# Optimization experiments

Hardware: AMD Instinct MI355X
Metric: run time of the kernel (lower is better)

The kernel has to match this reference:

```python
import jax, jax.numpy as jnp
import numpy as np

B, TQ, TK, DQ, DK = 8, 2048, 2048, 512, 512


def setup_inputs() -> dict:
    key = jax.random.key(0)
    kq, kk, kv, km, kw = jax.random.split(key, 5)
    q = jax.random.normal(kq, (B, TQ, DQ), dtype=jnp.float32)
    k = jax.random.normal(kk, (B, TK, DK), dtype=jnp.float32)
    v = jax.random.normal(kv, (B, TK, DK), dtype=jnp.float32)
    attn_mask = jax.random.randint(km, (B, TQ, TK), 0, 2) > 0
    # xavier_uniform for (DQ, DK)
    limit = float(np.sqrt(6.0 / (DQ + DK)))
    weights = jax.random.uniform(kw, (DQ, DK), minval=-limit, maxval=limit, dtype=jnp.float32)
    return {"q": q, "k": k, "v": v, "attn_mask": attn_mask, "weights": weights}


def reference(q, k, v, attn_mask, weights):
    # scores: (B, TQ, TK) = (q @ W) @ k^T
    qw = jnp.einsum('bqd,de->bqe', q, weights)
    scores = jnp.einsum('bqe,bke->bqk', qw, k)
    scores = jnp.where(attn_mask, -jnp.inf, scores)
    attention = jax.nn.softmax(scores, axis=-1)
    # dropout_rate = 0.0 -> identity
    output = jnp.einsum('bqk,bkd->bqd', attention, v)
    return (output, attention)
```

## Files before the change

### kernel.cpp

```cpp
#include <hip/hip_runtime.h>
#include <stdint.h>

#define TQs 2048
#define TKs 2048
#define DDs 512
#define NBs 8

typedef float f32x4 __attribute__((ext_vector_type(4)));
typedef float f32x2 __attribute__((ext_vector_type(2)));
typedef short bf16x8 __attribute__((ext_vector_type(8)));
typedef short bf16x4 __attribute__((ext_vector_type(4)));
typedef short bf16x2 __attribute__((ext_vector_type(2)));
typedef _Float16 half8 __attribute__((ext_vector_type(8)));

__device__ __forceinline__ unsigned short f2bf(float x){
  unsigned u = __float_as_uint(x);
  return (unsigned short)((u + 0x7fffu + ((u>>16)&1u)) >> 16);
}
__device__ __forceinline__ float bf2f(unsigned short h){
  return __uint_as_float(((unsigned)h)<<16);
}

__device__ __forceinline__ void gload16(const void* g, void* l){
  __builtin_amdgcn_global_load_lds(
      (const __attribute__((address_space(1))) unsigned int*)(unsigned long long)(uintptr_t)g,
      (__attribute__((address_space(3))) unsigned int*)(unsigned int)(uintptr_t)l,
      16, 0, 0);
}

__global__ __launch_bounds__(256) void k0_kf(const float* __restrict__ kk, _Float16* __restrict__ kf){
  const long n8 = (long)NBs*TKs*DDs/8;
  for(long i = (long)blockIdx.x*256 + threadIdx.x; i < n8; i += (long)gridDim.x*256){
    f32x4 x0 = ((const f32x4*)kk)[2*i];
    f32x4 x1 = ((const f32x4*)kk)[2*i+1];
    half8 h;
    #pragma unroll
    for(int j=0;j<4;j++){ h[j] = (_Float16)x0[j]; h[4+j] = (_Float16)x1[j]; }
    ((half8*)kf)[i] = h;
  }
}

__global__ __launch_bounds__(256) void k0_transpose_v(const float* __restrict__ v, short* __restrict__ vt){
  __shared__ float tile[64][65];
  int b = blockIdx.z;
  int t0 = blockIdx.x*64, d0 = blockIdx.y*64;
  int tid = threadIdx.x;
  int r = tid>>2, cs = (tid&3)*16;
  const float* src = v + ((long)b*TKs + t0 + r)*DDs + d0 + cs;
  #pragma unroll
  for(int i=0;i<4;i++){
    f32x4 x = ((const f32x4*)src)[i];
    tile[r][cs+4*i+0]=x[0]; tile[r][cs+4*i+1]=x[1]; tile[r][cs+4*i+2]=x[2]; tile[r][cs+4*i+3]=x[3];
  }
  __syncthreads();
  int dr = tid>>2, ts = (tid&3)*16;
  bf16x8 b0, b1;
  #pragma unroll
  for(int i=0;i<8;i++){ b0[i] = (short)f2bf(tile[ts+i][dr]); b1[i] = (short)f2bf(tile[ts+8+i][dr]); }
  short* dst = vt + ((long)b*DDs + d0 + dr)*TKs + t0 + ts;
  ((bf16x8*)dst)[0] = b0;
  ((bf16x8*)dst)[1] = b1;
}

__global__ __launch_bounds__(256) void k0_wt(const float* __restrict__ wsrc,
                                             short* __restrict__ wth, short* __restrict__ wtl){
  __shared__ float tile[64][65];
  int d0 = blockIdx.x*64, e0 = blockIdx.y*64;
  int tid = threadIdx.x;
  int r = tid>>2, cs = (tid&3)*16;
  const float* src = wsrc + ((long)(d0 + r))*DDs + e0 + cs;
  #pragma unroll
  for(int i=0;i<4;i++){
    f32x4 x = ((const f32x4*)src)[i];
    tile[r][cs+4*i+0]=x[0]; tile[r][cs+4*i+1]=x[1]; tile[r][cs+4*i+2]=x[2]; tile[r][cs+4*i+3]=x[3];
  }
  __syncthreads();
  int er = tid>>2, ds = (tid&3)*16;
  bf16x8 h0,h1,l0,l1;
  #pragma unroll
  for(int i=0;i<8;i++){
    float x = tile[ds+i][er];
    unsigned short hh = f2bf(x);
    h0[i] = (short)hh; l0[i] = (short)f2bf(x - bf2f(hh));
  }
  #pragma unroll
  for(int i=0;i<8;i++){
    float x = tile[ds+8+i][er];
    unsigned short hh = f2bf(x);
    h1[i] = (short)hh; l1[i] = (short)f2bf(x - bf2f(hh));
  }
  short* dh = wth + ((long)(e0+er))*DDs + d0 + ds;
  short* dl = wtl + ((long)(e0+er))*DDs + d0 + ds;
  ((bf16x8*)dh)[0] = h0; ((bf16x8*)dh)[1] = h1;
  ((bf16x8*)dl)[0] = l0; ((bf16x8*)dl)[1] = l1;
}

__global__ __launch_bounds__(256,2) void k1_qw(const float* __restrict__ q,
                                               const short* __restrict__ wth, const short* __restrict__ wtl,
                                               _Float16* __restrict__ qwh, _Float16* __restrict__ qwl){
  __shared__ short qah[8192], qal[8192];
  __shared__ short wbh[8192], wbl[8192];
  int q0 = blockIdx.x*128, e0 = blockIdx.y*128;
  int tid = threadIdx.x, lane = tid&63, w4 = tid>>6;
  int wm = w4>>1, wn = w4&1;
  int i15 = lane&15, g4 = lane>>4;
  f32x4 acc[4][4];
  #pragma unroll
  for(int a=0;a<4;a++)
    #pragma unroll
    for(int bq=0;bq<4;bq++) acc[a][bq] = (f32x4){0.f,0.f,0.f,0.f};
  for(int k0=0;k0<DDs;k0+=64){
    __syncthreads();
    #pragma unroll
    for(int j=0;j<4;j++){
      int J = j*4 + w4;
      long so = (long)(e0 + (J>>1)*16 + i15)*DDs + k0 + ((J&1)*4 + g4)*8;
      gload16(wth + so, &wbh[J*512]);
      gload16(wtl + so, &wbl[J*512]);
    }
    #pragma unroll
    for(int j=0;j<4;j++){
      int c = j*256 + tid;
      int ci = c&15, cg = (c>>4)&3, cks = (c>>6)&1, crb = c>>7;
      const float* s = q + (long)(q0 + crb*16 + ci)*DDs + k0 + (cks*4+cg)*8;
      f32x4 x0 = ((const f32x4*)s)[0];
      f32x4 x1 = ((const f32x4*)s)[1];
      bf16x8 h, l;
      #pragma unroll
      for(int jj=0;jj<4;jj++){
        unsigned short hj = f2bf(x0[jj]);
        h[jj] = (short)hj; l[jj] = (short)f2bf(x0[jj]-bf2f(hj));
      }
      #pragma unroll
      for(int jj=0;jj<4;jj++){
        unsigned short hj = f2bf(x1[jj]);
        h[4+jj] = (short)hj; l[4+jj] = (short)f2bf(x1[jj]-bf2f(hj));
      }
      *(bf16x8*)&qah[c*8] = h;
      *(bf16x8*)&qal[c*8] = l;
    }
    __syncthreads();
    #pragma unroll
    for(int ks=0;ks<2;ks++){
      bf16x8 a_h[4], a_l[4], b_h[4], b_l[4];
      #pragma unroll
      for(int mf=0;mf<4;mf++){
        int c = ((wm*4+mf)*2+ks)*64 + lane;
        a_h[mf] = *(const bf16x8*)&qah[c*8];
        a_l[mf] = *(const bf16x8*)&qal[c*8];
      }
      #pragma unroll
      for(int nf=0;nf<4;nf++){
        int c = ((wn*4+nf)*2+ks)*64 + lane;
        b_h[nf] = *(const bf16x8*)&wbh[c*8];
        b_l[nf] = *(const bf16x8*)&wbl[c*8];
      }
      #pragma unroll
      for(int mf=0;mf<4;mf++)
      #pragma unroll
      for(int nf=0;nf<4;nf++){
        acc[mf][nf] = __builtin_amdgcn_mfma_f32_16x16x32_bf16(a_h[mf], b_h[nf], acc[mf][nf],0,0,0);
        acc[mf][nf] = __builtin_amdgcn_mfma_f32_16x16x32_bf16(a_h[mf], b_l[nf], acc[mf][nf],0,0,0);
        acc[mf][nf] = __builtin_amdgcn_mfma_f32_16x16x32_bf16(a_l[mf], b_h[nf], acc[mf][nf],0,0,0);
      }
    }
  }
  int rr = g4*4, cc = i15;
  #pragma unroll
  for(int mf=0;mf<4;mf++)
  #pragma unroll
  for(int nf=0;nf<4;nf++)
  #pragma unroll
  for(int r2=0;r2<4;r2++){
    long row = q0 + wm*64 + mf*16 + rr + r2;
    long col = e0 + wn*64 + nf*16 + cc;
    float s = acc[mf][nf][r2];
    _Float16 h = (_Float16)s;
    qwh[row*DDs + col] = h;
    qwl[row*DDs + col] = (_Float16)(s - (float)h);
  }
}

__global__ __launch_bounds__(256,2) void k2a(const _Float16* __restrict__ qwh, const _Float16* __restrict__ qwl,
                                             const _Float16* __restrict__ kf,
                                             const int* __restrict__ mask, float* __restrict__ attn,
                                             float* __restrict__ m_ws, float* __restrict__ l_ws){
  __shared__ _Float16 kb[2][16384];
  int rb = blockIdx.x;
  int chunk = blockIdx.y;
  int tid = threadIdx.x, lane = tid&63, w = tid>>6;
  int b = rb>>5;
  long qrow0 = (long)rb*64 + w*16;
  int i15 = lane&15, g4 = lane>>4;
  half8 ah[16], al[16];
  {
    const _Float16* ph = qwh + (qrow0 + i15)*DDs + g4*8;
    const _Float16* pl = qwl + (qrow0 + i15)*DDs + g4*8;
    #pragma unroll
    for(int kc=0;kc<16;kc++){
      ah[kc] = *(const half8*)(ph + kc*32);
      al[kc] = *(const half8*)(pl + kc*32);
    }
  }
  float m_st[4], l_st[4];
  #pragma unroll
  for(int r=0;r<4;r++){ m_st[r]=-1e30f; l_st[r]=0.f; }
  const _Float16* kbase = kf + (long)b*TKs*DDs;
  {
    int t0 = chunk*1024;
    #pragma unroll
    for(int j=0;j<8;j++){
      int J = j*4 + w;
      long so = (long)(t0 + ((J>>4)<<4) + i15)*DDs + (J&15)*32 + g4*8;
      gload16(kbase + so, &kb[0][J*512]);
    }
  }
  __syncthreads();
  int cur = 0;
  for(int it=0; it<32; ++it){
    int t0 = chunk*1024 + it*32;
    if(it < 31){
      int t1 = t0 + 32;
      #pragma unroll
      for(int j=0;j<8;j++){
        int J = j*4 + w;
        long so = (long)(t1 + ((J>>4)<<4) + i15)*DDs + (J&15)*32 + g4*8;
        gload16(kbase + so, &kb[cur^1][J*512]);
      }
    }
    int mv[2][4];
    #pragma unroll
    for(int nf=0;nf<2;nf++)
      #pragma unroll
      for(int r=0;r<4;r++)
        mv[nf][r] = mask[(qrow0 + g4*4 + r)*TKs + t0 + nf*16 + i15];
    f32x4 acc[2];
    acc[0]=(f32x4){0.f,0.f,0.f,0.f}; acc[1]=(f32x4){0.f,0.f,0.f,0.f};
    #pragma unroll
    for(int ks=0;ks<16;ks++){
      #pragma unroll
      for(int nf=0;nf<2;nf++){
        half8 bh = *(const half8*)&kb[cur][((nf*16+ks)*64 + lane)*8];
        acc[nf] = __builtin_amdgcn_mfma_f32_16x16x32_f16(ah[ks], bh, acc[nf],0,0,0);
        acc[nf] = __builtin_amdgcn_mfma_f32_16x16x32_f16(al[ks], bh, acc[nf],0,0,0);
      }
    }
    #pragma unroll
    for(int r=0;r<4;r++){
      float s0 = acc[0][r];
      float s1 = acc[1][r];
      if(mv[0][r]) s0 = -3e38f;
      if(mv[1][r]) s1 = -3e38f;
      float mo = m_st[r];
      float mn = fmaxf(mo, fmaxf(s0,s1));
      l_st[r] = l_st[r]*__expf(mo-mn) + __expf(s0-mn) + __expf(s1-mn);
      m_st[r] = mn;
      long row = qrow0 + g4*4 + r;
      attn[row*TKs + t0 + i15] = s0;
      attn[row*TKs + t0 + 16 + i15] = s1;
    }
    __syncthreads();
    cur ^= 1;
  }
  #pragma unroll
  for(int r=0;r<4;r++){
    #pragma unroll
    for(int d=1; d<16; d<<=1){
      float m2 = __shfl_xor(m_st[r], d, 16);
      float l2 = __shfl_xor(l_st[r], d, 16);
      float mn = fmaxf(m_st[r], m2);
      l_st[r] = l_st[r]*__expf(m_st[r]-mn) + l2*__expf(m2-mn);
      m_st[r] = mn;
    }
  }
  if(i15==0){
    #pragma unroll
    for(int r=0;r<4;r++){
      long row = qrow0 + g4*4 + r;
      m_ws[row*2 + chunk] = m_st[r];
      l_ws[row*2 + chunk] = l_st[r];
    }
  }
}

__global__ __launch_bounds__(512,4) void k2b(const short* __restrict__ vt, const float* __restrict__ m_ws,
                                             const float* __restrict__ l_ws, float* __restrict__ attn,
                                             float* __restrict__ outp){
  __shared__ short vf[2][16384];
  __shared__ short at2[2][1024];
  __shared__ float ms[32], rls[32];
  int rb = blockIdx.x;
  long row0 = (long)rb*32;
  int b = rb>>6;
  int tid=threadIdx.x, lane=tid&63, w=tid>>6;
  int i15 = lane&15, g4 = lane>>4;
  const short* vb = vt + (long)b*DDs*TKs;
  float* arow = attn + row0*TKs;
  int nr = tid>>4, nt = (tid&15)*2;
  int nmf = nr>>4, nrow = nr&15, ntg = nt>>3, nj = nt&7;
  int ncell = (nmf*64 + ntg*16 + nrow)*8 + nj;
  #pragma unroll
  for(int j=0;j<4;j++){
    int J = j*8 + w;
    long so = (long)(J*16 + i15)*TKs + g4*8;
    gload16(vb + so, &vf[0][J*512]);
  }
  if(tid < 32){
    long row = row0 + tid;
    float m0=m_ws[row*2+0], m1=m_ws[row*2+1];
    float M = fmaxf(m0,m1);
    float L = l_ws[row*2+0]*__expf(m0-M) + l_ws[row*2+1]*__expf(m1-M);
    ms[tid] = M;
    rls[tid] = 1.0f/L;
  }
  __syncthreads();
  {
    float* p = arow + (long)nr*TKs + nt;
    f32x2 s = *(const f32x2*)p;
    float M = ms[nr], RL = rls[nr];
    float a0 = __expf(s[0]-M)*RL, a1 = __expf(s[1]-M)*RL;
    f32x2 av; av[0]=a0; av[1]=a1;
    *(f32x2*)p = av;
    bf16x2 ab; ab[0]=(short)f2bf(a0); ab[1]=(short)f2bf(a1);
    *(bf16x2*)&at2[0][ncell] = ab;
  }
  __syncthreads();
  f32x4 acc[2][4];
  #pragma unroll
  for(int mf=0;mf<2;mf++)
    #pragma unroll
    for(int nf=0;nf<4;nf++) acc[mf][nf]=(f32x4){0.f,0.f,0.f,0.f};
  int c = 0;
  for(int it=0; it<64; ++it){
    float sx, sy;
    if(it < 63){
      int t1 = (it+1)*32;
      #pragma unroll
      for(int j=0;j<4;j++){
        int J = j*8 + w;
        long so = (long)(J*16 + i15)*TKs + t1 + g4*8;
        gload16(vb + so, &vf[c^1][J*512]);
      }
      const float* p = arow + (long)nr*TKs + t1 + nt;
      f32x2 s = *(const f32x2*)p;
      sx = s[0]; sy = s[1];
    }
    bf16x8 af[2], bfr[4];
    #pragma unroll
    for(int mf=0;mf<2;mf++) af[mf] = *(const bf16x8*)&at2[c][(mf*64 + lane)*8];
    #pragma unroll
    for(int nf=0;nf<4;nf++) bfr[nf] = *(const bf16x8*)&vf[c][((w*4+nf)*64 + lane)*8];
    #pragma unroll
    for(int mf=0;mf<2;mf++)
    #pragma unroll
    for(int nf=0;nf<4;nf++)
      acc[mf][nf] = __builtin_amdgcn_mfma_f32_16x16x32_bf16(af[mf], bfr[nf], acc[mf][nf],0,0,0);
    if(it < 63){
      int t1 = (it+1)*32;
      float* p = arow + (long)nr*TKs + t1 + nt;
      float M = ms[nr], RL = rls[nr];
      float a0 = __expf(sx-M)*RL, a1 = __expf(sy-M)*RL;
      f32x2 av; av[0]=a0; av[1]=a1;
      *(f32x2*)p = av;
      bf16x2 ab; ab[0]=(short)f2bf(a0); ab[1]=(short)f2bf(a1);
      *(bf16x2*)&at2[c^1][ncell] = ab;
    }
    __syncthreads();
    c ^= 1;
  }
  #pragma unroll
  for(int mf=0;mf<2;mf++)
  #pragma unroll
  for(int nf=0;nf<4;nf++)
  #pragma unroll
  for(int r2=0;r2<4;r2++){
    long row = row0 + mf*16 + g4*4 + r2;
    long col = w*64 + nf*16 + i15;
    outp[row*DDs + col] = acc[mf][nf][r2];
  }
}

extern "C" void kernel_launch(void* const* d_in, const int* in_sizes, int n_in,
                              void* d_out, int out_size, void* d_ws, size_t ws_size,
                              hipStream_t stream) {
  const float* q    = (const float*)d_in[0];
  const float* k    = (const float*)d_in[1];
  const float* v    = (const float*)d_in[2];
  const int*   mask = (const int*)d_in[3];
  const float* wsrc = (const float*)d_in[4];
  float* outp = (float*)d_out;
  float* attn = (float*)d_out + (long)NBs*TQs*DDs;
  char* ws = (char*)d_ws;
  const long NE = (long)NBs*TKs*DDs;
  _Float16* kf  = (_Float16*)ws;
  short*    vt  = (short*)(ws + 2*NE);
  _Float16* qwh = (_Float16*)(ws + 4*NE);
  _Float16* qwl = (_Float16*)(ws + 6*NE);
  float* m_ws = (float*)(ws + 8*NE);
  float* l_ws = (float*)(ws + 8*NE + 65536*4);
  short* wth = (short*)attn;
  short* wtl = (short*)attn + 262144;
  hipLaunchKernelGGL(k0_kf,          dim3(1024),    dim3(256), 0, stream, k, kf);
  hipLaunchKernelGGL(k0_transpose_v, dim3(32,8,8),  dim3(256), 0, stream, v, vt);
  hipLaunchKernelGGL(k0_wt,          dim3(8,8),     dim3(256), 0, stream, wsrc, wth, wtl);
  hipLaunchKernelGGL(k1_qw,          dim3(128,4),   dim3(256), 0, stream, q, wth, wtl, qwh, qwl);
  hipLaunchKernelGGL(k2a,            dim3(256,2),   dim3(256), 0, stream, qwh, qwl, kf, mask, attn, m_ws, l_ws);
  hipLaunchKernelGGL(k2b,            dim3(512),     dim3(512), 0, stream, vt, m_ws, l_ws, attn, outp);
}
```

Before: 354.3 us.

## Prefetch mask and score tiles one iteration ahead and remap normalize threads

In the score kernel, the boolean mask values for the next K tile are loaded one iteration early into registers, so the mask read latency overlaps the MFMA work. In the normalize/PV kernel, the raw score pair for tile it+2 is prefetched into registers, which moves the global load off the critical path. The thread-to-element mapping is also changed so each wave writes a contiguous LDS region in the MFMA A-operand layout via a byte offset, replacing the scattered cell index. These changes cost extra registers and could lower occupancy.

```diff
diff --git a/kernel.cpp b/kernel.cpp
--- a/kernel.cpp
+++ b/kernel.cpp
@@ -206,6 +206,7 @@
   #pragma unroll
   for(int r=0;r<4;r++){ m_st[r]=-1e30f; l_st[r]=0.f; }
   const _Float16* kbase = kf + (long)b*TKs*DDs;
+  int mv_pf[2][4];
   {
     int t0 = chunk*1024;
     #pragma unroll
@@ -214,6 +215,11 @@
       long so = (long)(t0 + ((J>>4)<<4) + i15)*DDs + (J&15)*32 + g4*8;
       gload16(kbase + so, &kb[0][J*512]);
     }
+    #pragma unroll
+    for(int nf=0;nf<2;nf++)
+      #pragma unroll
+      for(int r=0;r<4;r++)
+        mv_pf[nf][r] = mask[(qrow0 + g4*4 + r)*TKs + t0 + nf*16 + i15];
   }
   __syncthreads();
   int cur = 0;
@@ -233,7 +239,15 @@
     for(int nf=0;nf<2;nf++)
       #pragma unroll
       for(int r=0;r<4;r++)
-        mv[nf][r] = mask[(qrow0 + g4*4 + r)*TKs + t0 + nf*16 + i15];
+        mv[nf][r] = mv_pf[nf][r];
+    if(it < 31){
+      int t1 = t0 + 32;
+      #pragma unroll
+      for(int nf=0;nf<2;nf++)
+        #pragma unroll
+        for(int r=0;r<4;r++)
+          mv_pf[nf][r] = mask[(qrow0 + g4*4 + r)*TKs + t1 + nf*16 + i15];
+    }
     f32x4 acc[2];
     acc[0]=(f32x4){0.f,0.f,0.f,0.f}; acc[1]=(f32x4){0.f,0.f,0.f,0.f};
     #pragma unroll
@@ -296,15 +310,16 @@
   int i15 = lane&15, g4 = lane>>4;
   const short* vb = vt + (long)b*DDs*TKs;
   float* arow = attn + row0*TKs;
-  int nr = tid>>4, nt = (tid&15)*2;
-  int nmf = nr>>4, nrow = nr&15, ntg = nt>>3, nj = nt&7;
-  int ncell = (nmf*64 + ntg*16 + nrow)*8 + nj;
+  int r_n = ((tid>>8)<<4) | (lane>>2);
+  int tn  = (((tid>>6)&3)<<3) | ((lane&3)<<1);
+  int nbyte = ((tid>>6)<<8) | (lane<<2);
   #pragma unroll
   for(int j=0;j<4;j++){
     int J = j*8 + w;
     long so = (long)(J*16 + i15)*TKs + g4*8;
     gload16(vb + so, &vf[0][J*512]);
   }
+  f32x2 s_pf = *(const f32x2*)(arow + (long)r_n*TKs + tn);
   if(tid < 32){
     long row = row0 + tid;
     float m0=m_ws[row*2+0], m1=m_ws[row*2+1];
@@ -315,15 +330,14 @@
   }
   __syncthreads();
   {
-    float* p = arow + (long)nr*TKs + nt;
-    f32x2 s = *(const f32x2*)p;
-    float M = ms[nr], RL = rls[nr];
-    float a0 = __expf(s[0]-M)*RL, a1 = __expf(s[1]-M)*RL;
+    float M = ms[r_n], RL = rls[r_n];
+    float a0 = __expf(s_pf[0]-M)*RL, a1 = __expf(s_pf[1]-M)*RL;
     f32x2 av; av[0]=a0; av[1]=a1;
-    *(f32x2*)p = av;
+    *(f32x2*)(arow + (long)r_n*TKs + tn) = av;
     bf16x2 ab; ab[0]=(short)f2bf(a0); ab[1]=(short)f2bf(a1);
-    *(bf16x2*)&at2[0][ncell] = ab;
-  }
+    *(bf16x2*)((char*)at2[0] + nbyte) = ab;
+  }
+  s_pf = *(const f32x2*)(arow + (long)r_n*TKs + 32 + tn);
   __syncthreads();
   f32x4 acc[2][4];
   #pragma unroll
@@ -332,7 +346,6 @@
     for(int nf=0;nf<4;nf++) acc[mf][nf]=(f32x4){0.f,0.f,0.f,0.f};
   int c = 0;
   for(int it=0; it<64; ++it){
-    float sx, sy;
     if(it < 63){
       int t1 = (it+1)*32;
       #pragma unroll
@@ -341,10 +354,10 @@
         long so = (long)(J*16 + i15)*TKs + t1 + g4*8;
         gload16(vb + so, &vf[c^1][J*512]);
       }
-      const float* p = arow + (long)nr*TKs + t1 + nt;
-      f32x2 s = *(const f32x2*)p;
-      sx = s[0]; sy = s[1];
-    }
+    }
+    f32x2 s_cur = s_pf;
+    if(it < 62)
+      s_pf = *(const f32x2*)(arow + (long)r_n*TKs + (it+2)*32 + tn);
     bf16x8 af[2], bfr[4];
     #pragma unroll
     for(int mf=0;mf<2;mf++) af[mf] = *(const bf16x8*)&at2[c][(mf*64 + lane)*8];
@@ -357,13 +370,12 @@
       acc[mf][nf] = __builtin_amdgcn_mfma_f32_16x16x32_bf16(af[mf], bfr[nf], acc[mf][nf],0,0,0);
     if(it < 63){
       int t1 = (it+1)*32;
-      float* p = arow + (long)nr*TKs + t1 + nt;
-      float M = ms[nr], RL = rls[nr];
-      float a0 = __expf(sx-M)*RL, a1 = __expf(sy-M)*RL;
+      float M = ms[r_n], RL = rls[r_n];
+      float a0 = __expf(s_cur[0]-M)*RL, a1 = __expf(s_cur[1]-M)*RL;
       f32x2 av; av[0]=a0; av[1]=a1;
-      *(f32x2*)p = av;
+      *(f32x2*)(arow + (long)r_n*TKs + t1 + tn) = av;
       bf16x2 ab; ab[0]=(short)f2bf(a0); ab[1]=(short)f2bf(a1);
-      *(bf16x2*)&at2[c^1][ncell] = ab;
+      *(bf16x2*)((char*)at2[c^1] + nbyte) = ab;
     }
     __syncthreads();
     c ^= 1;
```

Measured after the change: 349.1 us. About the same (-1.5%).
